# Kernel tuning notes

Hardware: AMD Instinct MI355X
Metric: run time of the kernel (lower is better)

The kernel has to match this reference:

```python
import jax, jax.numpy as jnp
import numpy as np

SCALE = 0.02  # init scale for weight matrices


def setup_inputs() -> dict:
    B, M, H = 2048, 64, 1024
    key = jax.random.key(0)
    ks = jax.random.split(key, 10)
    inp = {
        "pose_embed": jax.random.normal(ks[0], (B, H), jnp.float32),
        "query_embed": jax.random.normal(ks[1], (B, H), jnp.float32),
        "h": jax.random.normal(ks[2], (B, H), jnp.float32),
        "c": jax.random.normal(ks[3], (B, H), jnp.float32),
        "memory": jax.random.normal(ks[4], (B, M, H), jnp.float32),
        "W_ih": jax.random.normal(ks[5], (4 * H, H), jnp.float32) * SCALE,
        "W_hh": jax.random.normal(ks[6], (4 * H, H), jnp.float32) * SCALE,
        "b_ih": jnp.zeros((4 * H,), jnp.float32),
        "b_hh": jnp.zeros((4 * H,), jnp.float32),
        "Wq": jax.random.normal(ks[7], (H, H), jnp.float32) * SCALE,
        "bq": jnp.zeros((H,), jnp.float32),
        "Wk": jax.random.normal(ks[8], (H, H), jnp.float32) * SCALE,
        "bk": jnp.zeros((H,), jnp.float32),
        "Wv": jax.random.normal(ks[9], (H, H), jnp.float32) * SCALE,
        "bv": jnp.zeros((H,), jnp.float32),
    }
    return inp


def reference(pose_embed, query_embed, h, c, memory,
              W_ih, W_hh, b_ih, b_hh, Wq, bq, Wk, bk, Wv, bv):
    H = pose_embed.shape[-1]
    # --- LSTMCell step (torch gate order: i, f, g, o) ---
    gates = pose_embed @ W_ih.T + b_ih + h @ W_hh.T + b_hh  # [B, 4H]
    i_g, f_g, g_g, o_g = jnp.split(gates, 4, axis=-1)
    c_new = jax.nn.sigmoid(f_g) * c + jax.nn.sigmoid(i_g) * jnp.tanh(g_g)
    h_new = jax.nn.sigmoid(o_g) * jnp.tanh(c_new)
    # --- FIFO memory update (detach, pop oldest, append new h) ---
    mem = jnp.concatenate(
        [memory[:, 1:], jax.lax.stop_gradient(h_new)[:, None]], axis=1)  # [B, M, H]
    # --- single-query attention over memory ---
    Q = query_embed @ Wq.T + bq                       # [B, H]
    K = mem @ Wk.T + bk                               # [B, M, H]
    V = mem @ Wv.T + bv                               # [B, M, H]
    scores = jnp.einsum('bh,bmh->bm', Q, K) / jnp.sqrt(jnp.float32(H))
    attn = jax.nn.softmax(scores, axis=-1)            # [B, M]
    attended = jnp.einsum('bm,bmh->bh', attn, V)      # [B, H]
    return attended, h_new, c_new
```

## Files before the change

### kernel.cpp

```cpp
#include <hip/hip_runtime.h>
#include <stdint.h>

typedef __attribute__((ext_vector_type(8))) short short8;
typedef __attribute__((ext_vector_type(4))) float f32x4;
typedef unsigned short u16;

__device__ __forceinline__ u16 f2bf(float f) {
  union { float f; uint32_t u; } v; v.f = f;
  return (u16)((v.u + 0x7FFFu + ((v.u >> 16) & 1u)) >> 16);
}
__device__ __forceinline__ float bf2f(u16 u) {
  union { uint32_t u; float f; } v; v.u = (uint32_t)u << 16; return v.f;
}

__device__ __forceinline__ void gl_lds16(const void* g, void* l) {
  __builtin_amdgcn_global_load_lds(
      (const __attribute__((address_space(1))) void*)g,
      (__attribute__((address_space(3))) void*)l, 16, 0, 0);
}

__global__ __launch_bounds__(256) void gemm_bt(
    const u16* __restrict__ A, const u16* __restrict__ B,
    float* __restrict__ Cf, u16* __restrict__ Cb,
    const float* __restrict__ bias1,
    int M, int N, int K)
{
  __shared__ __align__(16) u16 As[128 * 32];
  __shared__ __align__(16) u16 Bs[128 * 32];
  const int t = threadIdx.x;
  const int lane = t & 63;
  const int w = t >> 6;
  const int wr = w >> 1, wc = w & 1;
  const int m0 = blockIdx.y * 128, n0 = blockIdx.x * 128;
  const int lr = lane & 15;
  const int lk = (lane >> 4) * 8;
  const int srow = t >> 2;
  const int scol = (t & 3) * 8;

  const u16* gA = A + (size_t)(m0 + srow) * K + scol;
  const u16* gB = B + (size_t)(n0 + srow) * K + scol;

  f32x4 acc[4][4] = {};

  for (int k0 = 0; k0 < K; k0 += 32) {
    gl_lds16(gA,                  As + t * 8);
    gl_lds16(gA + (size_t)64 * K, As + 2048 + t * 8);
    gl_lds16(gB,                  Bs + t * 8);
    gl_lds16(gB + (size_t)64 * K, Bs + 2048 + t * 8);
    gA += 32; gB += 32;
    __syncthreads();

    short8 a[4], b[4];
#pragma unroll
    for (int m = 0; m < 4; ++m)
      a[m] = *(const short8*)(As + (wr * 64 + m * 16 + lr) * 32 + lk);
#pragma unroll
    for (int n = 0; n < 4; ++n)
      b[n] = *(const short8*)(Bs + (wc * 64 + n * 16 + lr) * 32 + lk);
#pragma unroll
    for (int m = 0; m < 4; ++m)
#pragma unroll
      for (int n = 0; n < 4; ++n)
        acc[m][n] = __builtin_amdgcn_mfma_f32_16x16x32_bf16(a[m], b[n], acc[m][n], 0, 0, 0);
    __syncthreads();
  }

#pragma unroll
  for (int n = 0; n < 4; ++n) {
    int col = n0 + wc * 64 + n * 16 + lr;
    float bsum = bias1 ? bias1[col] : 0.f;
#pragma unroll
    for (int m = 0; m < 4; ++m) {
#pragma unroll
      for (int r = 0; r < 4; ++r) {
        int row = m0 + wr * 64 + m * 16 + (lane >> 4) * 4 + r;
        float vv = acc[m][n][r] + bsum;
        if (Cf) Cf[(size_t)row * N + col] = vv;
        if (Cb) Cb[(size_t)row * N + col] = f2bf(vv);
      }
    }
  }
}

__global__ __launch_bounds__(256) void gates_k(
    const u16* __restrict__ Xcat, const u16* __restrict__ Wcat,
    u16* __restrict__ gates,
    const float* __restrict__ b_ih, const float* __restrict__ b_hh)
{
  __shared__ __align__(16) u16 As[128 * 32];
  __shared__ __align__(16) u16 Bs[128 * 32];
  const int t = threadIdx.x;
  const int lane = t & 63;
  const int gid = blockIdx.x;
  const int m0 = (gid >> 5) * 128, n0 = (gid & 31) * 128;
  const int w = t >> 6;
  const int wr = w >> 1, wc = w & 1;
  const int lr = lane & 15;
  const int lk = (lane >> 4) * 8;
  const int srow = t >> 2;
  const int scol = (t & 3) * 8;

  const u16* gA = Xcat + (size_t)(m0 + srow) * 2048 + scol;
  const u16* gB = Wcat + (size_t)(n0 + srow) * 2048 + scol;

  f32x4 acc[4][4] = {};
  for (int k0 = 0; k0 < 2048; k0 += 32) {
    gl_lds16(gA,                     As + t * 8);
    gl_lds16(gA + (size_t)64 * 2048, As + 2048 + t * 8);
    gl_lds16(gB,                     Bs + t * 8);
    gl_lds16(gB + (size_t)64 * 2048, Bs + 2048 + t * 8);
    gA += 32; gB += 32;
    __syncthreads();
    short8 a[4], b[4];
#pragma unroll
    for (int m = 0; m < 4; ++m)
      a[m] = *(const short8*)(As + (wr * 64 + m * 16 + lr) * 32 + lk);
#pragma unroll
    for (int n = 0; n < 4; ++n)
      b[n] = *(const short8*)(Bs + (wc * 64 + n * 16 + lr) * 32 + lk);
#pragma unroll
    for (int m = 0; m < 4; ++m)
#pragma unroll
      for (int n = 0; n < 4; ++n)
        acc[m][n] = __builtin_amdgcn_mfma_f32_16x16x32_bf16(a[m], b[n], acc[m][n], 0, 0, 0);
    __syncthreads();
  }
#pragma unroll
  for (int n = 0; n < 4; ++n) {
    int col = n0 + wc * 64 + n * 16 + lr;
    float bsum = b_ih[col] + b_hh[col];
#pragma unroll
    for (int m = 0; m < 4; ++m)
#pragma unroll
      for (int r = 0; r < 4; ++r) {
        int row = m0 + wr * 64 + m * 16 + (lane >> 4) * 4 + r;
        gates[(size_t)row * 4096 + col] = f2bf(acc[m][n][r] + bsum);
      }
  }
}

__global__ __launch_bounds__(256) void attn_k(
    const float* __restrict__ Qk, const float* __restrict__ mem,
    float* __restrict__ attst)
{
  const int t = threadIdx.x;
  const int lane = t & 63;
  const int b = blockIdx.x * 4 + (t >> 6);
  const float* q = Qk + (size_t)b * 1024;
  f32x4 qv[4];
#pragma unroll
  for (int i = 0; i < 4; ++i)
    qv[i] = *(const f32x4*)(q + (i * 64 + lane) * 4);
  const float* mb = mem + (size_t)b * 65536;

  float m_run = -3e38f, l = 0.f;
  f32x4 cx[4] = {};

  for (int qd = 0; qd < 15; ++qd) {
    const float* r0 = mb + (size_t)(1 + qd * 4) * 1024;
    f32x4 rv[4][4];
    float s[4] = {0.f, 0.f, 0.f, 0.f};
#pragma unroll
    for (int rr = 0; rr < 4; ++rr)
#pragma unroll
      for (int i = 0; i < 4; ++i) {
        rv[rr][i] = __builtin_nontemporal_load(
            (const f32x4*)(r0 + rr * 1024 + (i * 64 + lane) * 4));
        s[rr] += rv[rr][i][0] * qv[i][0] + rv[rr][i][1] * qv[i][1] +
                 rv[rr][i][2] * qv[i][2] + rv[rr][i][3] * qv[i][3];
      }
#pragma unroll
    for (int rr = 0; rr < 4; ++rr) {
#pragma unroll
      for (int off = 32; off; off >>= 1) s[rr] += __shfl_xor(s[rr], off);
      s[rr] *= 0.03125f;
    }
#pragma unroll
    for (int rr = 0; rr < 4; ++rr) {
      if (s[rr] <= m_run + 8.f) {
        float e = __expf(s[rr] - m_run);
        l += e;
#pragma unroll
        for (int i = 0; i < 4; ++i) cx[i] += rv[rr][i] * e;
      } else {
        float sc = __expf(m_run - s[rr]);
        m_run = s[rr];
        l = l * sc + 1.f;
#pragma unroll
        for (int i = 0; i < 4; ++i) cx[i] = cx[i] * sc + rv[rr][i];
      }
    }
  }
  for (int r = 61; r <= 63; ++r) {
    const float* row = mb + (size_t)r * 1024;
    f32x4 rv[4];
    float s = 0.f;
#pragma unroll
    for (int i = 0; i < 4; ++i) {
      rv[i] = __builtin_nontemporal_load(
          (const f32x4*)(row + (i * 64 + lane) * 4));
      s += rv[i][0] * qv[i][0] + rv[i][1] * qv[i][1] +
           rv[i][2] * qv[i][2] + rv[i][3] * qv[i][3];
    }
#pragma unroll
    for (int off = 32; off; off >>= 1) s += __shfl_xor(s, off);
    s *= 0.03125f;
    if (s <= m_run + 8.f) {
      float e = __expf(s - m_run);
      l += e;
#pragma unroll
      for (int i = 0; i < 4; ++i) cx[i] += rv[i] * e;
    } else {
      float sc = __expf(m_run - s);
      m_run = s;
      l = l * sc + 1.f;
#pragma unroll
      for (int i = 0; i < 4; ++i) cx[i] = cx[i] * sc + rv[i];
    }
  }
  float* st = attst + (size_t)b * 1032;
#pragma unroll
  for (int i = 0; i < 4; ++i)
    *(f32x4*)(st + (i * 64 + lane) * 4) = cx[i];
  if (lane == 0) { st[1024] = m_run; st[1025] = l; }
}

__global__ __launch_bounds__(256) void prep_k(
    const float* __restrict__ pose, const float* __restrict__ h,
    const float* __restrict__ W_ih, const float* __restrict__ W_hh,
    const float* __restrict__ query, const float* __restrict__ Wv,
    const float* __restrict__ Wq, const float* __restrict__ Wk,
    u16* __restrict__ xcat, u16* __restrict__ wcat,
    u16* __restrict__ qry, u16* __restrict__ wvb,
    u16* __restrict__ wqtb, u16* __restrict__ wktb)
{
  __shared__ u16 tile[64][65];
  int blk = blockIdx.x;
  int t = threadIdx.x;
  if (blk >= 15360) {
    const float* src; u16* dst; int tblk;
    if (blk < 15616) { src = Wq; dst = wqtb; tblk = blk - 15360; }
    else             { src = Wk; dst = wktb; tblk = blk - 15616; }
    int tr = (tblk >> 4) * 64, tc = (tblk & 15) * 64;
    int tx = t & 63;
    int ty = (t >> 6) * 16;
#pragma unroll
    for (int i = 0; i < 16; ++i)
      tile[ty + i][tx] = f2bf(src[(size_t)(tr + ty + i) * 1024 + tc + tx]);
    __syncthreads();
#pragma unroll
    for (int i = 0; i < 16; ++i)
      dst[(size_t)(tc + ty + i) * 1024 + tr + tx] = tile[tx][ty + i];
    return;
  }
  const float* src; u16* dst; int ostride, ooff, base;
  if (blk < 2048)       { src = pose;  dst = xcat; ostride = 2048; ooff = 0;    base = 0; }
  else if (blk < 4096)  { src = h;     dst = xcat; ostride = 2048; ooff = 1024; base = 2048; }
  else if (blk < 8192)  { src = W_ih;  dst = wcat; ostride = 2048; ooff = 0;    base = 4096; }
  else if (blk < 12288) { src = W_hh;  dst = wcat; ostride = 2048; ooff = 1024; base = 8192; }
  else if (blk < 14336) { src = query; dst = qry;  ostride = 1024; ooff = 0;    base = 12288; }
  else                  { src = Wv;    dst = wvb;  ostride = 1024; ooff = 0;    base = 14336; }
  int r = blk - base;
  int cc = t * 4;
  float4 v = *(const float4*)(src + (size_t)r * 1024 + cc);
  ushort4 o; o.x = f2bf(v.x); o.y = f2bf(v.y); o.z = f2bf(v.z); o.w = f2bf(v.w);
  *(ushort4*)(dst + (size_t)r * ostride + ooff + cc) = o;
}

__global__ __launch_bounds__(256) void bqwk_k(
    const float* __restrict__ bq, const float* __restrict__ Wk,
    float* __restrict__ qkb)
{
  int n = blockIdx.x * 256 + threadIdx.x;
  int j0 = blockIdx.y * 64;
  float s = 0.f;
#pragma unroll 8
  for (int j = j0; j < j0 + 64; ++j) s += bq[j] * Wk[(size_t)j * 1024 + n];
  atomicAdd(&qkb[n], s);
}

__global__ __launch_bounds__(256) void lstmfin_k(
    const u16* __restrict__ gates, const float* __restrict__ c,
    const float* __restrict__ Qk, const float* __restrict__ attst,
    float* __restrict__ out_h, float* __restrict__ out_c,
    u16* __restrict__ ctxb)
{
  const int b = blockIdx.x;
  const int t = threadIdx.x;
  const int lane = t & 63, wv_id = t >> 6;
  const int p = t * 4;
  const u16* g = gates + (size_t)b * 4096;
  ushort4 igu = *(const ushort4*)(g + p);
  ushort4 fgu = *(const ushort4*)(g + 1024 + p);
  ushort4 ggu = *(const ushort4*)(g + 2048 + p);
  ushort4 ogu = *(const ushort4*)(g + 3072 + p);
  float4 cv = *(const float4*)(c + (size_t)b * 1024 + p);

  float hn[4], cn[4];
  {
    float igs[4] = {bf2f(igu.x), bf2f(igu.y), bf2f(igu.z), bf2f(igu.w)};
    float fgs[4] = {bf2f(fgu.x), bf2f(fgu.y), bf2f(fgu.z), bf2f(fgu.w)};
    float ggs[4] = {bf2f(ggu.x), bf2f(ggu.y), bf2f(ggu.z), bf2f(ggu.w)};
    float ogs[4] = {bf2f(ogu.x), bf2f(ogu.y), bf2f(ogu.z), bf2f(ogu.w)};
    float cvs[4] = {cv.x, cv.y, cv.z, cv.w};
#pragma unroll
    for (int j = 0; j < 4; ++j) {
      float si = 1.f / (1.f + __expf(-igs[j]));
      float sf = 1.f / (1.f + __expf(-fgs[j]));
      float so = 1.f / (1.f + __expf(-ogs[j]));
      float tg = 2.f / (1.f + __expf(-2.f * ggs[j])) - 1.f;
      cn[j] = sf * cvs[j] + si * tg;
      float tc2 = 2.f / (1.f + __expf(-2.f * cn[j])) - 1.f;
      hn[j] = so * tc2;
    }
  }
  *(float4*)(out_c + (size_t)b * 1024 + p) = make_float4(cn[0], cn[1], cn[2], cn[3]);
  *(float4*)(out_h + (size_t)b * 1024 + p) = make_float4(hn[0], hn[1], hn[2], hn[3]);

  float4 qv = *(const float4*)(Qk + (size_t)b * 1024 + p);
  float part = qv.x * hn[0] + qv.y * hn[1] + qv.z * hn[2] + qv.w * hn[3];
#pragma unroll
  for (int off = 32; off; off >>= 1) part += __shfl_xor(part, off);
  __shared__ float red[4];
  if (lane == 0) red[wv_id] = part;
  __syncthreads();
  float s_last = (red[0] + red[1] + red[2] + red[3]) * 0.03125f;

  const float* st = attst + (size_t)b * 1032;
  float m_run = st[1024], l = st[1025];
  float4 cx = *(const float4*)(st + p);
  if (s_last <= m_run + 8.f) {
    float e = __expf(s_last - m_run);
    l += e;
    cx.x += e * hn[0]; cx.y += e * hn[1]; cx.z += e * hn[2]; cx.w += e * hn[3];
  } else {
    float sc = __expf(m_run - s_last);
    l = l * sc + 1.f;
    cx.x = cx.x * sc + hn[0]; cx.y = cx.y * sc + hn[1];
    cx.z = cx.z * sc + hn[2]; cx.w = cx.w * sc + hn[3];
  }
  float inv = 1.f / l;
  ushort4 o;
  o.x = f2bf(cx.x * inv); o.y = f2bf(cx.y * inv);
  o.z = f2bf(cx.z * inv); o.w = f2bf(cx.w * inv);
  *(ushort4*)(ctxb + (size_t)b * 1024 + p) = o;
}

extern "C" void kernel_launch(void* const* d_in, const int* in_sizes, int n_in,
                              void* d_out, int out_size, void* d_ws, size_t ws_size,
                              hipStream_t stream) {
  const int Bb = 2048, Hh = 1024;
  const float* pose  = (const float*)d_in[0];
  const float* query = (const float*)d_in[1];
  const float* h     = (const float*)d_in[2];
  const float* c     = (const float*)d_in[3];
  const float* mem   = (const float*)d_in[4];
  const float* W_ih  = (const float*)d_in[5];
  const float* W_hh  = (const float*)d_in[6];
  const float* b_ih  = (const float*)d_in[7];
  const float* b_hh  = (const float*)d_in[8];
  const float* Wq    = (const float*)d_in[9];
  const float* bq    = (const float*)d_in[10];
  const float* Wk    = (const float*)d_in[11];
  const float* Wv    = (const float*)d_in[13];
  const float* bv    = (const float*)d_in[14];

  float* out_att = (float*)d_out;
  float* out_h   = out_att + (size_t)Bb * Hh;
  float* out_c   = out_h + (size_t)Bb * Hh;

  char* wp = (char*)d_ws;
  auto alloc = [&](size_t bytes) {
    char* p = wp; wp += (bytes + 255) & ~(size_t)255; return p;
  };
  u16*   Xcat  = (u16*)alloc((size_t)2048 * 2048 * 2);
  u16*   Wcat  = (u16*)alloc((size_t)4096 * 2048 * 2);
  u16*   Qryb  = (u16*)alloc((size_t)2048 * 1024 * 2);
  u16*   WqTb  = (u16*)alloc((size_t)1024 * 1024 * 2);
  u16*   WkTb  = (u16*)alloc((size_t)1024 * 1024 * 2);
  u16*   Gb    = (u16*)alloc((size_t)1024 * 1024 * 2);
  u16*   Wvb   = (u16*)alloc((size_t)1024 * 1024 * 2);
  u16*   gates = (u16*)alloc((size_t)2048 * 4096 * 2);
  float* qkb   = (float*)alloc((size_t)1024 * 4);
  float* Qk    = (float*)alloc((size_t)2048 * 1024 * 4);
  u16*   ctxb  = (u16*)alloc((size_t)2048 * 1024 * 2);
  float* attst = (float*)Qryb;

  prep_k<<<15872, 256, 0, stream>>>(pose, h, W_ih, W_hh, query, Wv, Wq, Wk,
                                    Xcat, Wcat, Qryb, Wvb, WqTb, WkTb);

  hipMemsetAsync(qkb, 0, 1024 * sizeof(float), stream);
  bqwk_k<<<dim3(4, 16), 256, 0, stream>>>(bq, Wk, qkb);

  gemm_bt<<<dim3(8, 8), 256, 0, stream>>>(
      WkTb, WqTb, nullptr, Gb, nullptr, 1024, 1024, 1024);

  gemm_bt<<<dim3(8, 16), 256, 0, stream>>>(
      Qryb, Gb, Qk, nullptr, qkb, 2048, 1024, 1024);

  gates_k<<<512, 256, 0, stream>>>(Xcat, Wcat, gates, b_ih, b_hh);

  attn_k<<<512, 256, 0, stream>>>(Qk, mem, attst);

  lstmfin_k<<<2048, 256, 0, stream>>>(gates, c, Qk, attst, out_h, out_c, ctxb);

  gemm_bt<<<dim3(8, 16), 256, 0, stream>>>(
      ctxb, Wvb, out_att, nullptr, bv, 2048, 1024, 1024);
}
```

Before: 248.1 us.

## Double-buffer GEMM LDS tiles with async prefetch and merge gates GEMM into generic kernel

The generic bf16 GEMM now uses two LDS buffers. The next k-tile is prefetched with global_load_lds while the current one feeds MFMA, using explicit vmcnt waits, sched barriers and setprio around the MFMA block. Bias loads are hoisted before the loop, and a second bias pointer is added. The dedicated gates kernel is removed, and the LSTM gates GEMM now runs through the same pipelined kernel. This aims to hide global load latency behind compute, at the cost of double the LDS footprint, which may limit occupancy.

After: 267.1 us. 7.7% more time.

```diff
diff --git a/kernel.cpp b/kernel.cpp
--- a/kernel.cpp
+++ b/kernel.cpp
@@ -4,6 +4,12 @@
 typedef __attribute__((ext_vector_type(8))) short short8;
 typedef __attribute__((ext_vector_type(4))) float f32x4;
 typedef unsigned short u16;
+
+#define VMCNT4() asm volatile("s_waitcnt vmcnt(4)" ::: "memory")
+#define VMCNT0() asm volatile("s_waitcnt vmcnt(0)" ::: "memory")
+#define SBAR() do { __builtin_amdgcn_sched_barrier(0); \
+                    __builtin_amdgcn_s_barrier(); \
+                    __builtin_amdgcn_sched_barrier(0); } while (0)
 
 __device__ __forceinline__ u16 f2bf(float f) {
   union { float f; uint32_t u; } v; v.f = f;
@@ -22,11 +28,11 @@
 __global__ __launch_bounds__(256) void gemm_bt(
     const u16* __restrict__ A, const u16* __restrict__ B,
     float* __restrict__ Cf, u16* __restrict__ Cb,
-    const float* __restrict__ bias1,
+    const float* __restrict__ bias1, const float* __restrict__ bias2,
     int M, int N, int K)
 {
-  __shared__ __align__(16) u16 As[128 * 32];
-  __shared__ __align__(16) u16 Bs[128 * 32];
+  __shared__ __align__(16) u16 As[2][128 * 32];
+  __shared__ __align__(16) u16 Bs[2][128 * 32];
   const int t = threadIdx.x;
   const int lane = t & 63;
   const int w = t >> 6;
@@ -37,105 +43,71 @@
   const int srow = t >> 2;
   const int scol = (t & 3) * 8;
 
+  float bs[4];
+#pragma unroll
+  for (int n = 0; n < 4; ++n) {
+    int col = n0 + wc * 64 + n * 16 + lr;
+    float v = 0.f;
+    if (bias1) v += bias1[col];
+    if (bias2) v += bias2[col];
+    bs[n] = v;
+  }
+  VMCNT0();
+
   const u16* gA = A + (size_t)(m0 + srow) * K + scol;
   const u16* gB = B + (size_t)(n0 + srow) * K + scol;
+  const int nt = K >> 5;
+
+  auto STAGE = [&](int buf) {
+    gl_lds16(gA,                 As[buf] + t * 8);
+    gl_lds16(gA + (size_t)64 * K, As[buf] + 2048 + t * 8);
+    gl_lds16(gB,                 Bs[buf] + t * 8);
+    gl_lds16(gB + (size_t)64 * K, Bs[buf] + 2048 + t * 8);
+    gA += 32; gB += 32;
+  };
 
   f32x4 acc[4][4] = {};
 
-  for (int k0 = 0; k0 < K; k0 += 32) {
-    gl_lds16(gA,                  As + t * 8);
-    gl_lds16(gA + (size_t)64 * K, As + 2048 + t * 8);
-    gl_lds16(gB,                  Bs + t * 8);
-    gl_lds16(gB + (size_t)64 * K, Bs + 2048 + t * 8);
-    gA += 32; gB += 32;
-    __syncthreads();
-
+  STAGE(0);
+  STAGE(1);
+  VMCNT4();
+  SBAR();
+
+  for (int tt = 0; tt < nt; ++tt) {
+    const int cur = tt & 1;
     short8 a[4], b[4];
 #pragma unroll
     for (int m = 0; m < 4; ++m)
-      a[m] = *(const short8*)(As + (wr * 64 + m * 16 + lr) * 32 + lk);
+      a[m] = *(const short8*)(As[cur] + (wr * 64 + m * 16 + lr) * 32 + lk);
 #pragma unroll
     for (int n = 0; n < 4; ++n)
-      b[n] = *(const short8*)(Bs + (wc * 64 + n * 16 + lr) * 32 + lk);
+      b[n] = *(const short8*)(Bs[cur] + (wc * 64 + n * 16 + lr) * 32 + lk);
+    __builtin_amdgcn_s_setprio(1);
 #pragma unroll
     for (int m = 0; m < 4; ++m)
 #pragma unroll
       for (int n = 0; n < 4; ++n)
         acc[m][n] = __builtin_amdgcn_mfma_f32_16x16x32_bf16(a[m], b[n], acc[m][n], 0, 0, 0);
-    __syncthreads();
+    __builtin_amdgcn_s_setprio(0);
+    SBAR();
+    if (tt + 2 < nt) { STAGE(cur); VMCNT4(); }
+    else             { VMCNT0(); }
+    SBAR();
   }
 
 #pragma unroll
   for (int n = 0; n < 4; ++n) {
     int col = n0 + wc * 64 + n * 16 + lr;
-    float bsum = bias1 ? bias1[col] : 0.f;
 #pragma unroll
     for (int m = 0; m < 4; ++m) {
 #pragma unroll
       for (int r = 0; r < 4; ++r) {
         int row = m0 + wr * 64 + m * 16 + (lane >> 4) * 4 + r;
-        float vv = acc[m][n][r] + bsum;
+        float vv = acc[m][n][r] + bs[n];
         if (Cf) Cf[(size_t)row * N + col] = vv;
         if (Cb) Cb[(size_t)row * N + col] = f2bf(vv);
       }
     }
-  }
-}
-
-__global__ __launch_bounds__(256) void gates_k(
-    const u16* __restrict__ Xcat, const u16* __restrict__ Wcat,
-    u16* __restrict__ gates,
-    const float* __restrict__ b_ih, const float* __restrict__ b_hh)
-{
-  __shared__ __align__(16) u16 As[128 * 32];
-  __shared__ __align__(16) u16 Bs[128 * 32];
-  const int t = threadIdx.x;
-  const int lane = t & 63;
-  const int gid = blockIdx.x;
-  const int m0 = (gid >> 5) * 128, n0 = (gid & 31) * 128;
-  const int w = t >> 6;
-  const int wr = w >> 1, wc = w & 1;
-  const int lr = lane & 15;
-  const int lk = (lane >> 4) * 8;
-  const int srow = t >> 2;
-  const int scol = (t & 3) * 8;
-
-  const u16* gA = Xcat + (size_t)(m0 + srow) * 2048 + scol;
-  const u16* gB = Wcat + (size_t)(n0 + srow) * 2048 + scol;
-
-  f32x4 acc[4][4] = {};
-  for (int k0 = 0; k0 < 2048; k0 += 32) {
-    gl_lds16(gA,                     As + t * 8);
-    gl_lds16(gA + (size_t)64 * 2048, As + 2048 + t * 8);
-    gl_lds16(gB,                     Bs + t * 8);
-    gl_lds16(gB + (size_t)64 * 2048, Bs + 2048 + t * 8);
-    gA += 32; gB += 32;
-    __syncthreads();
-    short8 a[4], b[4];
-#pragma unroll
-    for (int m = 0; m < 4; ++m)
-      a[m] = *(const short8*)(As + (wr * 64 + m * 16 + lr) * 32 + lk);
-#pragma unroll
-    for (int n = 0; n < 4; ++n)
-      b[n] = *(const short8*)(Bs + (wc * 64 + n * 16 + lr) * 32 + lk);
-#pragma unroll
-    for (int m = 0; m < 4; ++m)
-#pragma unroll
-      for (int n = 0; n < 4; ++n)
-        acc[m][n] = __builtin_amdgcn_mfma_f32_16x16x32_bf16(a[m], b[n], acc[m][n], 0, 0, 0);
-    __syncthreads();
-  }
-#pragma unroll
-  for (int n = 0; n < 4; ++n) {
-    int col = n0 + wc * 64 + n * 16 + lr;
-    float bsum = b_ih[col] + b_hh[col];
-#pragma unroll
-    for (int m = 0; m < 4; ++m)
-#pragma unroll
-      for (int r = 0; r < 4; ++r) {
-        int row = m0 + wr * 64 + m * 16 + (lane >> 4) * 4 + r;
-        gates[(size_t)row * 4096 + col] = f2bf(acc[m][n][r] + bsum);
-      }
   }
 }
 
@@ -393,17 +365,18 @@
   bqwk_k<<<dim3(4, 16), 256, 0, stream>>>(bq, Wk, qkb);
 
   gemm_bt<<<dim3(8, 8), 256, 0, stream>>>(
-      WkTb, WqTb, nullptr, Gb, nullptr, 1024, 1024, 1024);
+      WkTb, WqTb, nullptr, Gb, nullptr, nullptr, 1024, 1024, 1024);
 
   gemm_bt<<<dim3(8, 16), 256, 0, stream>>>(
-      Qryb, Gb, Qk, nullptr, qkb, 2048, 1024, 1024);
-
-  gates_k<<<512, 256, 0, stream>>>(Xcat, Wcat, gates, b_ih, b_hh);
+      Qryb, Gb, Qk, nullptr, qkb, nullptr, 2048, 1024, 1024);
+
+  gemm_bt<<<dim3(32, 16), 256, 0, stream>>>(
+      Xcat, Wcat, nullptr, gates, b_ih, b_hh, 2048, 4096, 2048);
 
   attn_k<<<512, 256, 0, stream>>>(Qk, mem, attst);
 
   lstmfin_k<<<2048, 256, 0, stream>>>(gates, c, Qk, attst, out_h, out_c, ctxb);
 
   gemm_bt<<<dim3(8, 16), 256, 0, stream>>>(
-      ctxb, Wvb, out_att, nullptr, bv, 2048, 1024, 1024);
-}
+      ctxb, Wvb, out_att, nullptr, bv, nullptr, 2048, 1024, 1024);
+}
```
